# Performance work log

Hardware: AMD Instinct MI355X
Metric: run time of the kernel (lower is better)

Reference implementation:

```python
import jax, jax.numpy as jnp
import numpy as np

N = 50000
E = 400000
DIM_IN = 512
DIM_H = 64
HEADS = 8
DIM_OUT = 40
SLOPE = 0.2  # PyG GATv2Conv default negative_slope


def setup_inputs() -> dict:
    key = jax.random.key(0)
    ks = jax.random.split(key, 16)
    s = 0.05
    return {
        "x": jax.random.normal(ks[0], (N, DIM_IN), dtype=jnp.float32),
        "edge_index": jax.random.randint(ks[1], (2, E), 0, N, dtype=jnp.int64),
        "Wl1": jax.random.normal(ks[2], (DIM_IN, HEADS * DIM_H), dtype=jnp.float32) * s,
        "Wr1": jax.random.normal(ks[3], (DIM_IN, HEADS * DIM_H), dtype=jnp.float32) * s,
        "att1": jax.random.normal(ks[4], (HEADS, DIM_H), dtype=jnp.float32) * s,
        "b1": jax.random.normal(ks[5], (HEADS * DIM_H,), dtype=jnp.float32) * s,
        "Wl2": jax.random.normal(ks[6], (HEADS * DIM_H, DIM_OUT), dtype=jnp.float32) * s,
        "Wr2": jax.random.normal(ks[7], (HEADS * DIM_H, DIM_OUT), dtype=jnp.float32) * s,
        "att2": jax.random.normal(ks[8], (1, DIM_OUT), dtype=jnp.float32) * s,
        "b2": jax.random.normal(ks[9], (DIM_OUT,), dtype=jnp.float32) * s,
        "Wl3": jax.random.normal(ks[10], (HEADS * DIM_H, 2), dtype=jnp.float32) * s,
        "Wr3": jax.random.normal(ks[11], (HEADS * DIM_H, 2), dtype=jnp.float32) * s,
        "att3": jax.random.normal(ks[12], (1, 2), dtype=jnp.float32) * s,
        "b3": jax.random.normal(ks[13], (2,), dtype=jnp.float32) * s,
    }


def gatv2(x, src, dst, Wl, Wr, att, b):
    # PyG GATv2Conv: e_ij = att . LeakyReLU(W_l x_j + W_r x_i); softmax over j (by dst i);
    # out_i = sum_j alpha_ij * (W_l x_j); heads concatenated; bias added after.
    n = x.shape[0]
    H, F = att.shape
    xl = (x @ Wl).reshape(n, H, F)  # source transform
    xr = (x @ Wr).reshape(n, H, F)  # target transform
    e = jax.nn.leaky_relu(xl[src] + xr[dst], negative_slope=SLOPE)  # [E, H, F]
    logits = jnp.einsum("ehf,hf->eh", e, att)  # [E, H]
    m = jax.ops.segment_max(logits, dst, num_segments=n)  # self-loops => every segment nonempty
    ex = jnp.exp(logits - m[dst])
    denom = jax.ops.segment_sum(ex, dst, num_segments=n)
    alpha = ex / denom[dst]  # [E, H]
    out = jax.ops.segment_sum(xl[src] * alpha[:, :, None], dst, num_segments=n)  # [N, H, F]
    return out.reshape(n, H * F) + b


def reference(x, edge_index, Wl1, Wr1, att1, b1, Wl2, Wr2, att2, b2, Wl3, Wr3, att3, b3):
    # add self loops (PyG default add_self_loops=True)
    loops = jnp.arange(N, dtype=edge_index.dtype)
    ei = jnp.concatenate([edge_index, jnp.stack([loops, loops])], axis=1)
    src, dst = ei[0], ei[1]
    # eval mode: dropout is identity; ReverseLayerF is identity in forward
    h = jax.nn.relu(gatv2(x, src, dst, Wl1, Wr1, att1, b1))
    y_class = gatv2(h, src, dst, Wl2, Wr2, att2, b2)
    y_domain = gatv2(h, src, dst, Wl3, Wr3, att3, b3)
    return (y_class, y_domain)
```

## Files before the change

### kernel.cpp

```cpp
#include <hip/hip_runtime.h>
#include <math.h>

typedef unsigned short u16;
typedef unsigned int   u32;
typedef __attribute__((ext_vector_type(8))) short bf16x8;
typedef __attribute__((ext_vector_type(4))) float f32x4;
typedef __attribute__((ext_vector_type(4))) u32   u32x4;

__device__ __forceinline__ float b2f(u16 u) {
  union { u32 i; float f; } v; v.i = ((u32)u) << 16; return v.f;
}
__device__ __forceinline__ u16 f2b(float f) {
  union { u32 i; float f; } v; v.f = f;
  u32 r = v.i + 0x7FFFu + ((v.i >> 16) & 1u);
  return (u16)(r >> 16);
}
__device__ __forceinline__ float blo(u32 w) {
  union { u32 i; float f; } v; v.i = w << 16; return v.f;
}
__device__ __forceinline__ float bhi(u32 w) {
  union { u32 i; float f; } v; v.i = w & 0xFFFF0000u; return v.f;
}
__device__ __forceinline__ void ld_lds16(const u16* g, u16* l) {
  __builtin_amdgcn_global_load_lds((const __attribute__((address_space(1))) void*)g,
                                   (__attribute__((address_space(3))) void*)l, 16, 0, 0);
}

#define NN 50000
#define NE 400000
#define NT 450000
#define NBLK_SCAN 196

__global__ void k_detect(const void* x, const void* ei, int* flags) {
  __shared__ int cnt[2];
  int t = threadIdx.x;
  if (t < 2) cnt[t] = 0;
  __syncthreads();
  u16 u = ((const u16*)x)[t];
  int e = (u >> 7) & 0xFF;
  if (u == 0 || (e >= 90 && e <= 134)) atomicAdd(&cnt[0], 1);
  if (t < 16) {
    if (((const int*)ei)[2 * t + 1] == 0) atomicAdd(&cnt[1], 1);
  }
  __syncthreads();
  if (t == 0) {
    flags[0] = (cnt[0] >= 110) ? 1 : 0;
    flags[1] = (cnt[1] >= 15) ? 1 : 0;
  }
}

__device__ __forceinline__ int eidx(const int* ei, int pos, int i64) {
  return i64 ? ei[2 * pos] : ei[pos];
}

__global__ void k_convert_x(const void* x, const int* flags, u16* xb) {
  if (flags[0]) return;
  int c = blockIdx.x * 256 + threadIdx.x;
  const float* xf = (const float*)x + (size_t)c * 8;
  u32x4 o;
  #pragma unroll
  for (int i = 0; i < 4; ++i) {
    u32 lo = f2b(xf[2 * i]);
    u32 hi = f2b(xf[2 * i + 1]);
    o[i] = lo | (hi << 16);
  }
  *(u32x4*)(xb + (size_t)c * 8) = o;
}

__global__ void k_pack_w1t(const void* Wl1, const void* Wr1, const int* flags, u16* w1t) {
  int t = blockIdx.x * 256 + threadIdx.x;
  int k = t >> 10;
  int c = t & 1023;
  const void* W = (c < 512) ? Wl1 : Wr1;
  int cc = c & 511;
  u16 v;
  if (flags[0]) v = ((const u16*)W)[k * 512 + cc];
  else          v = f2b(((const float*)W)[k * 512 + cc]);
  w1t[c * 512 + k] = v;
}

__global__ void k_pack_w23t(const void* Wl2, const void* Wr2, const void* Wl3, const void* Wr3,
                            const int* flags, u16* w23t) {
  int t = blockIdx.x * 256 + threadIdx.x;
  int k = t / 96;
  int c = t % 96;
  const void* W = nullptr; int idx = 0;
  if (c < 40)      { W = Wl2; idx = k * 40 + c; }
  else if (c < 42) { W = Wl3; idx = k * 2 + (c - 40); }
  else if (c < 82) { W = Wr2; idx = k * 40 + (c - 42); }
  else if (c < 84) { W = Wr3; idx = k * 2 + (c - 82); }
  u16 v = 0;
  if (W) {
    if (flags[0]) v = ((const u16*)W)[idx];
    else          v = f2b(((const float*)W)[idx]);
  }
  w23t[c * 512 + k] = v;
}

__global__ void k_pack_params(const void* att1, const void* b1, const void* att2, const void* b2,
                              const void* att3, const void* b3, const int* flags, float* params) {
  int t = blockIdx.x * 256 + threadIdx.x;
  if (t >= 1108) return;
  const void* src; int idx;
  if (t < 512)       { src = att1; idx = t; }
  else if (t < 1024) { src = b1;   idx = t - 512; }
  else if (t < 1064) { src = att2; idx = t - 1024; }
  else if (t < 1104) { src = b2;   idx = t - 1064; }
  else if (t < 1106) { src = att3; idx = t - 1104; }
  else               { src = b3;   idx = t - 1106; }
  params[t] = flags[0] ? b2f(((const u16*)src)[idx]) : ((const float*)src)[idx];
}

__global__ void k_hist(const int* ei, const int* flags, int* deg) {
  int e = blockIdx.x * 256 + threadIdx.x;
  if (e >= NE) return;
  int d = eidx(ei, NE + e, flags[1]);
  atomicAdd(&deg[d], 1);
}

__global__ void k_scanA(const int* deg, int* row_ptr, int* bsum) {
  __shared__ int sh[256];
  int b = blockIdx.x, t = threadIdx.x;
  int i = b * 256 + t;
  int val = (i < NN) ? deg[i] + 1 : 0;
  sh[t] = val;
  __syncthreads();
  #pragma unroll
  for (int off = 1; off < 256; off <<= 1) {
    int v = (t >= off) ? sh[t - off] : 0;
    __syncthreads();
    sh[t] += v;
    __syncthreads();
  }
  if (i < NN) row_ptr[i] = sh[t] - val;
  if (t == 255) bsum[b] = sh[255];
}

__global__ void k_scanB(int* bsum, int* row_ptr) {
  __shared__ int sh[256];
  int t = threadIdx.x;
  int val = (t < NBLK_SCAN) ? bsum[t] : 0;
  sh[t] = val;
  __syncthreads();
  #pragma unroll
  for (int off = 1; off < 256; off <<= 1) {
    int v = (t >= off) ? sh[t - off] : 0;
    __syncthreads();
    sh[t] += v;
    __syncthreads();
  }
  if (t < NBLK_SCAN) bsum[t] = sh[t] - val;
  if (t == 255) row_ptr[NN] = sh[255];
}

__global__ void k_scanC(const int* bsum, int* row_ptr, int* cursor) {
  int i = blockIdx.x * 256 + threadIdx.x;
  if (i < NN) {
    int v = row_ptr[i] + bsum[blockIdx.x];
    row_ptr[i] = v;
    cursor[i] = v;
  }
}

__global__ void k_scatter(const int* ei, const int* flags, int* cursor, int* csr_src) {
  int t = blockIdx.x * 256 + threadIdx.x;
  if (t >= NT) return;
  int i64 = flags[1];
  int s, d;
  if (t < NE) { s = eidx(ei, t, i64); d = eidx(ei, NE + t, i64); }
  else        { s = d = t - NE; }
  int pos = atomicAdd(&cursor[d], 1);
  csr_src[pos] = s;
}

__global__ __launch_bounds__(256) void k_gemm1(const void* __restrict__ xraw, const u16* __restrict__ xb,
                                               const u16* __restrict__ Bt, const int* __restrict__ flags,
                                               u16* __restrict__ XL, u16* __restrict__ XR) {
  __shared__ __align__(16) u16 As[128 * 32];
  __shared__ __align__(16) u16 Bs[128 * 32];
  const int id  = blockIdx.x;
  const int xcd = id & 7;
  const int lb  = id >> 3;
  const int mt  = xcd * 49 + (lb >> 3);
  const int nt  = lb & 7;
  if (mt >= 391) return;
  const int m0 = mt * 128;
  const int n0 = nt * 128;
  const u16* __restrict__ A = flags[0] ? (const u16*)xraw : xb;
  const int t = threadIdx.x;
  const int wave = t >> 6;
  const int lane = t & 63;
  const int wm = (wave >> 1) * 64;
  const int wn = (wave & 1) * 64;
  const int fr = lane & 15;
  const int fk = lane >> 4;
  const int rsub = lane >> 2;
  const int achk = ((lane & 3) + (rsub >> 1)) & 3;
  const int sA = ((fk - (fr >> 1)) & 3) * 8;
  f32x4 acc[4][4] = {};
  for (int k0 = 0; k0 < 512; k0 += 32) {
    #pragma unroll
    for (int c = 0; c < 2; ++c) {
      int rbase = wave * 16 + c * 64;
      int gm = m0 + rbase + rsub;
      if (gm > NN - 1) gm = NN - 1;
      ld_lds16(&A[(size_t)gm * 512 + k0 + achk * 8], &As[rbase * 32]);
      ld_lds16(&Bt[(size_t)(n0 + rbase + rsub) * 512 + k0 + achk * 8], &Bs[rbase * 32]);
    }
    __syncthreads();
    bf16x8 af[4], bb[4];
    #pragma unroll
    for (int i = 0; i < 4; ++i) af[i] = *(const bf16x8*)&As[(wm + i * 16 + fr) * 32 + sA];
    #pragma unroll
    for (int j = 0; j < 4; ++j) bb[j] = *(const bf16x8*)&Bs[(wn + j * 16 + fr) * 32 + sA];
    #pragma unroll
    for (int i = 0; i < 4; ++i)
      #pragma unroll
      for (int j = 0; j < 4; ++j)
        acc[i][j] = __builtin_amdgcn_mfma_f32_16x16x32_bf16(af[i], bb[j], acc[i][j], 0, 0, 0);
    __syncthreads();
  }
  #pragma unroll
  for (int i = 0; i < 4; ++i) {
    #pragma unroll
    for (int r = 0; r < 4; ++r) {
      int gm = m0 + wm + i * 16 + fk * 4 + r;
      if (gm < NN) {
        #pragma unroll
        for (int j = 0; j < 4; ++j) {
          int gn = n0 + wn + j * 16 + fr;
          u16 v = f2b(acc[i][j][r]);
          if (gn < 512) XL[(size_t)gm * 512 + gn] = v;
          else          XR[(size_t)gm * 512 + gn - 512] = v;
        }
      }
    }
  }
}

__global__ __launch_bounds__(256) void k_gemm2(const u16* __restrict__ A, const u16* __restrict__ Bt,
                                               float* __restrict__ C) {
  __shared__ __align__(16) short As[128][40];
  __shared__ __align__(16) short Bs[96][40];
  const int m0 = blockIdx.x * 128;
  const int t = threadIdx.x;
  const int wave = t >> 6;
  const int lane = t & 63;
  const int fr = lane & 15;
  const int fk = lane >> 4;
  const int wm = wave * 32;
  f32x4 acc[2][6] = {};
  for (int k0 = 0; k0 < 512; k0 += 32) {
    #pragma unroll
    for (int h = 0; h < 2; ++h) {
      int c = t + h * 256;
      int row = c >> 2, kc = (c & 3) * 8;
      int gm = m0 + row;
      u32x4 va = {0, 0, 0, 0};
      if (gm < NN) va = *(const u32x4*)&A[(size_t)gm * 512 + k0 + kc];
      *(u32x4*)&As[row][kc] = va;
    }
    for (int c = t; c < 384; c += 256) {
      int row = c >> 2, kc = (c & 3) * 8;
      *(u32x4*)&Bs[row][kc] = *(const u32x4*)&Bt[row * 512 + k0 + kc];
    }
    __syncthreads();
    bf16x8 af[2], bb[6];
    #pragma unroll
    for (int i = 0; i < 2; ++i) af[i] = *(const bf16x8*)&As[wm + i * 16 + fr][fk * 8];
    #pragma unroll
    for (int j = 0; j < 6; ++j) bb[j] = *(const bf16x8*)&Bs[j * 16 + fr][fk * 8];
    #pragma unroll
    for (int i = 0; i < 2; ++i)
      #pragma unroll
      for (int j = 0; j < 6; ++j)
        acc[i][j] = __builtin_amdgcn_mfma_f32_16x16x32_bf16(af[i], bb[j], acc[i][j], 0, 0, 0);
    __syncthreads();
  }
  #pragma unroll
  for (int i = 0; i < 2; ++i) {
    #pragma unroll
    for (int j = 0; j < 6; ++j) {
      int gn = j * 16 + fr;
      if (gn < 84) {
        #pragma unroll
        for (int r = 0; r < 4; ++r) {
          int gm = m0 + wm + i * 16 + fk * 4 + r;
          if (gm < NN) C[(size_t)gm * 84 + gn] = acc[i][j][r];
        }
      }
    }
  }
}

__global__ __launch_bounds__(256) void k_layer1f(const u16* __restrict__ xl1, const u16* __restrict__ xr1,
                                                 const int* __restrict__ row_ptr, const int* __restrict__ csr_src,
                                                 const float* __restrict__ params, u16* __restrict__ hb) {
  int wid = blockIdx.x * 4 + (threadIdx.x >> 6);
  int lane = threadIdx.x & 63;
  int nw = gridDim.x * 4;
  float att[8];
  #pragma unroll
  for (int k = 0; k < 8; ++k) att[k] = params[lane * 8 + k];
  for (int i = wid; i < NN; i += nw) {
    int e0 = row_ptr[i], e1 = row_ptr[i + 1];
    u32x4 xrv = *(const u32x4*)&xr1[(size_t)i * 512 + lane * 8];
    float xr[8];
    #pragma unroll
    for (int q = 0; q < 4; ++q) { xr[2 * q] = blo(xrv[q]); xr[2 * q + 1] = bhi(xrv[q]); }
    float s = 0.f;
    float acc[8] = {0.f, 0.f, 0.f, 0.f, 0.f, 0.f, 0.f, 0.f};
    for (int p = e0; p < e1; p += 4) {
      int p1 = p + 1 < e1 ? p + 1 : e1 - 1;
      int p2 = p + 2 < e1 ? p + 2 : e1 - 1;
      int p3 = p + 3 < e1 ? p + 3 : e1 - 1;
      int j0 = csr_src[p], j1 = csr_src[p1], j2 = csr_src[p2], j3 = csr_src[p3];
      u32x4 v0 = *(const u32x4*)&xl1[(size_t)j0 * 512 + lane * 8];
      u32x4 v1 = *(const u32x4*)&xl1[(size_t)j1 * 512 + lane * 8];
      u32x4 v2 = *(const u32x4*)&xl1[(size_t)j2 * 512 + lane * 8];
      u32x4 v3 = *(const u32x4*)&xl1[(size_t)j3 * 512 + lane * 8];
      float m1 = (p + 1 < e1) ? 1.f : 0.f;
      float m2 = (p + 2 < e1) ? 1.f : 0.f;
      float m3 = (p + 3 < e1) ? 1.f : 0.f;
      float c0 = 0.f, c1 = 0.f, c2 = 0.f, c3 = 0.f;
      float xlv0[8], xlv1[8], xlv2[8], xlv3[8];
      #pragma unroll
      for (int q = 0; q < 4; ++q) {
        xlv0[2 * q] = blo(v0[q]); xlv0[2 * q + 1] = bhi(v0[q]);
        xlv1[2 * q] = blo(v1[q]); xlv1[2 * q + 1] = bhi(v1[q]);
        xlv2[2 * q] = blo(v2[q]); xlv2[2 * q + 1] = bhi(v2[q]);
        xlv3[2 * q] = blo(v3[q]); xlv3[2 * q + 1] = bhi(v3[q]);
      }
      #pragma unroll
      for (int k = 0; k < 8; ++k) {
        float t0 = xlv0[k] + xr[k];
        float t1 = xlv1[k] + xr[k];
        float t2 = xlv2[k] + xr[k];
        float t3 = xlv3[k] + xr[k];
        c0 = fmaf(att[k], fmaxf(t0, 0.2f * t0), c0);
        c1 = fmaf(att[k], fmaxf(t1, 0.2f * t1), c1);
        c2 = fmaf(att[k], fmaxf(t2, 0.2f * t2), c2);
        c3 = fmaf(att[k], fmaxf(t3, 0.2f * t3), c3);
      }
      c0 += __shfl_xor(c0, 1, 64); c1 += __shfl_xor(c1, 1, 64);
      c2 += __shfl_xor(c2, 1, 64); c3 += __shfl_xor(c3, 1, 64);
      c0 += __shfl_xor(c0, 2, 64); c1 += __shfl_xor(c1, 2, 64);
      c2 += __shfl_xor(c2, 2, 64); c3 += __shfl_xor(c3, 2, 64);
      c0 += __shfl_xor(c0, 4, 64); c1 += __shfl_xor(c1, 4, 64);
      c2 += __shfl_xor(c2, 4, 64); c3 += __shfl_xor(c3, 4, 64);
      float pv0 = __expf(fminf(fmaxf(c0, -30.f), 30.f));
      float pv1 = __expf(fminf(fmaxf(c1, -30.f), 30.f)) * m1;
      float pv2 = __expf(fminf(fmaxf(c2, -30.f), 30.f)) * m2;
      float pv3 = __expf(fminf(fmaxf(c3, -30.f), 30.f)) * m3;
      s += (pv0 + pv1) + (pv2 + pv3);
      #pragma unroll
      for (int k = 0; k < 8; ++k) {
        float a = fmaf(pv0, xlv0[k], pv1 * xlv1[k]);
        float b = fmaf(pv2, xlv2[k], pv3 * xlv3[k]);
        acc[k] += a + b;
      }
    }
    float r = 1.f / s;
    u32x4 o;
    #pragma unroll
    for (int q = 0; q < 4; ++q) {
      u32 lo = f2b(fmaxf(fmaf(acc[2 * q],     r, params[512 + lane * 8 + 2 * q]),     0.f));
      u32 hi = f2b(fmaxf(fmaf(acc[2 * q + 1], r, params[512 + lane * 8 + 2 * q + 1]), 0.f));
      o[q] = lo | (hi << 16);
    }
    *(u32x4*)&hb[(size_t)i * 512 + lane * 8] = o;
  }
}

__global__ __launch_bounds__(256) void k_layer23f(const float* __restrict__ xlr23, const int* __restrict__ row_ptr,
                                                  const int* __restrict__ csr_src, const float* __restrict__ params,
                                                  const int* __restrict__ flags, void* __restrict__ out) {
  int wid = blockIdx.x * 4 + (threadIdx.x >> 6);
  int lane = threadIdx.x & 63;
  int nw = gridDim.x * 4;
  int c = lane;
  bool act = c < 42;
  float att = 0.f;
  if (c < 40)      att = params[1024 + c];
  else if (c < 42) att = params[1104 + (c - 40)];
  int isbf = flags[0];
  for (int i = wid; i < NN; i += nw) {
    int e0 = row_ptr[i], e1 = row_ptr[i + 1];
    float xr = act ? xlr23[(size_t)i * 84 + 42 + c] : 0.f;
    float s2 = 0.f, s3 = 0.f, acc = 0.f;
    for (int p = e0; p < e1; p += 2) {
      int p1 = p + 1 < e1 ? p + 1 : e1 - 1;
      float m1 = (p + 1 < e1) ? 1.f : 0.f;
      int j0 = csr_src[p], j1 = csr_src[p1];
      float xl0 = act ? xlr23[(size_t)j0 * 84 + c] : 0.f;
      float xl1 = act ? xlr23[(size_t)j1 * 84 + c] : 0.f;
      float t0 = xl0 + xr, t1 = xl1 + xr;
      float v0 = att * fmaxf(t0, 0.2f * t0);
      float v1 = att * fmaxf(t1, 0.2f * t1);
      float w0 = (c < 40) ? v0 : 0.f;
      float w1 = (c < 40) ? v1 : 0.f;
      #pragma unroll
      for (int o = 32; o >= 1; o >>= 1) { w0 += __shfl_xor(w0, o, 64); w1 += __shfl_xor(w1, o, 64); }
      float u0 = v0 + __shfl_xor(v0, 1, 64);
      float u1 = v1 + __shfl_xor(v1, 1, 64);
      float l3_0 = __shfl(u0, 40, 64);
      float l3_1 = __shfl(u1, 40, 64);
      float p2_0 = __expf(fminf(fmaxf(w0, -30.f), 30.f));
      float p2_1 = __expf(fminf(fmaxf(w1, -30.f), 30.f)) * m1;
      float p3_0 = __expf(fminf(fmaxf(l3_0, -30.f), 30.f));
      float p3_1 = __expf(fminf(fmaxf(l3_1, -30.f), 30.f)) * m1;
      s2 += p2_0 + p2_1;
      s3 += p3_0 + p3_1;
      float a0 = (c < 40) ? p2_0 : p3_0;
      float a1 = (c < 40) ? p2_1 : p3_1;
      acc += fmaf(a0, xl0, a1 * xl1);
    }
    if (c < 40) {
      float v = acc / s2 + params[1064 + c];
      size_t o = (size_t)i * 40 + c;
      if (isbf) ((u16*)out)[o] = f2b(v); else ((float*)out)[o] = v;
    } else if (c < 42) {
      float v = acc / s3 + params[1106 + (c - 40)];
      size_t o = 2000000 + (size_t)i * 2 + (c - 40);
      if (isbf) ((u16*)out)[o] = f2b(v); else ((float*)out)[o] = v;
    }
  }
}

extern "C" void kernel_launch(void* const* d_in, const int* in_sizes, int n_in,
                              void* d_out, int out_size, void* d_ws, size_t ws_size,
                              hipStream_t stream) {
  const void* x    = d_in[0];
  const int*  ei   = (const int*)d_in[1];
  const void* Wl1  = d_in[2];
  const void* Wr1  = d_in[3];
  const void* att1 = d_in[4];
  const void* b1   = d_in[5];
  const void* Wl2  = d_in[6];
  const void* Wr2  = d_in[7];
  const void* att2 = d_in[8];
  const void* b2   = d_in[9];
  const void* Wl3  = d_in[10];
  const void* Wr3  = d_in[11];
  const void* att3 = d_in[12];
  const void* b3   = d_in[13];
  (void)in_sizes; (void)n_in; (void)out_size;

  char* ws = (char*)d_ws;
  size_t off = 0;
  auto alloc = [&](size_t bytes) -> void* {
    void* p = ws + off;
    off = (off + bytes + 255) & ~(size_t)255;
    return p;
  };
  int*   flags   = (int*)  alloc(64);
  u16*   xb      = (u16*)  alloc((size_t)NN * 512 * 2);
  u16*   w1t     = (u16*)  alloc((size_t)1024 * 512 * 2);
  u16*   xl1     = (u16*)  alloc((size_t)NN * 512 * 2);
  u16*   xr1     = (u16*)  alloc((size_t)NN * 512 * 2);
  u16*   hb      = (u16*)  alloc((size_t)NN * 512 * 2);
  u16*   w23t    = (u16*)  alloc((size_t)96 * 512 * 2);
  float* xlr23   = (float*)alloc((size_t)NN * 84 * 4);
  float* params  = (float*)alloc(1108 * 4);
  int*   row_ptr = (int*)  alloc((NN + 1) * 4);
  int*   deg     = (int*)  alloc(NN * 4);
  int*   cursor  = (int*)  alloc(NN * 4);
  int*   csr_src = (int*)  alloc((NT + 16) * 4);
  int*   bsum    = (int*)  alloc(256 * 4);
  if (ws_size < off) return;

  hipLaunchKernelGGL(k_detect, dim3(1), dim3(128), 0, stream, x, (const void*)ei, flags);
  hipLaunchKernelGGL(k_convert_x, dim3(12500), dim3(256), 0, stream, x, flags, xb);
  hipLaunchKernelGGL(k_pack_w1t, dim3(2048), dim3(256), 0, stream, Wl1, Wr1, flags, w1t);
  hipLaunchKernelGGL(k_pack_w23t, dim3(192), dim3(256), 0, stream, Wl2, Wr2, Wl3, Wr3, flags, w23t);
  hipLaunchKernelGGL(k_pack_params, dim3(5), dim3(256), 0, stream, att1, b1, att2, b2, att3, b3, flags, params);
  hipMemsetAsync(deg, 0, NN * 4, stream);
  hipLaunchKernelGGL(k_hist, dim3((NE + 255) / 256), dim3(256), 0, stream, ei, flags, deg);
  hipLaunchKernelGGL(k_scanA, dim3(NBLK_SCAN), dim3(256), 0, stream, deg, row_ptr, bsum);
  hipLaunchKernelGGL(k_scanB, dim3(1), dim3(256), 0, stream, bsum, row_ptr);
  hipLaunchKernelGGL(k_scanC, dim3(NBLK_SCAN), dim3(256), 0, stream, bsum, row_ptr, cursor);
  hipLaunchKernelGGL(k_scatter, dim3((NT + 255) / 256), dim3(256), 0, stream, ei, flags, cursor, csr_src);
  hipLaunchKernelGGL(k_gemm1, dim3(3136), dim3(256), 0, stream, x, xb, w1t, flags, xl1, xr1);
  hipLaunchKernelGGL(k_layer1f, dim3(4096), dim3(256), 0, stream, xl1, xr1, row_ptr, csr_src, params, hb);
  hipLaunchKernelGGL(k_gemm2, dim3(391), dim3(256), 0, stream, hb, w23t, xlr23);
  hipLaunchKernelGGL(k_layer23f, dim3(4096), dim3(256), 0, stream, xlr23, row_ptr, csr_src, params, flags, d_out);
}
```

Baseline: 479.5 us.

## Fuse prep kernels, inline dtype detection, single-block scan, bf16 layer-2 features

Merges input conversion, weight packing, parameter packing and degree zeroing into one kernel. Dtype and index-width detection move into each kernel via wave ballots, replacing the flags buffer. The three-pass scan becomes one 1024-thread block. gemm1 keeps B fragments in registers with a 64-wide K step, and the layer-2/3 projection buffer is stored as bf16 to halve gather bandwidth. This trades some precision in the final layers and serialises the scan on one block.

After: 626.8 us. +30.7%, slower.

```diff
diff --git a/kernel.cpp b/kernel.cpp
--- a/kernel.cpp
+++ b/kernel.cpp
@@ -26,158 +26,154 @@
                                    (__attribute__((address_space(3))) void*)l, 16, 0, 0);
 }
 
+__device__ __forceinline__ int is_bf16_w(const void* x) {
+  int lane = threadIdx.x & 63;
+  u32 w = ((const u32*)x)[lane];
+  u16 a = (u16)(w & 0xFFFF), b = (u16)(w >> 16);
+  int ea = (a >> 7) & 0xFF, eb = (b >> 7) & 0xFF;
+  bool oka = (a == 0) || (ea >= 90 && ea <= 134);
+  bool okb = (b == 0) || (eb >= 90 && eb <= 134);
+  int cnt = (int)__popcll(__ballot(oka)) + (int)__popcll(__ballot(okb));
+  return cnt >= 110;
+}
+__device__ __forceinline__ int is_i64_w(const int* ei) {
+  int lane = threadIdx.x & 63;
+  int v = (lane < 16) ? (ei[2 * lane + 1] == 0) : 0;
+  return (int)__popcll(__ballot(v)) >= 15;
+}
+
 #define NN 50000
 #define NE 400000
 #define NT 450000
-#define NBLK_SCAN 196
-
-__global__ void k_detect(const void* x, const void* ei, int* flags) {
-  __shared__ int cnt[2];
-  int t = threadIdx.x;
-  if (t < 2) cnt[t] = 0;
-  __syncthreads();
-  u16 u = ((const u16*)x)[t];
-  int e = (u >> 7) & 0xFF;
-  if (u == 0 || (e >= 90 && e <= 134)) atomicAdd(&cnt[0], 1);
-  if (t < 16) {
-    if (((const int*)ei)[2 * t + 1] == 0) atomicAdd(&cnt[1], 1);
-  }
-  __syncthreads();
-  if (t == 0) {
-    flags[0] = (cnt[0] >= 110) ? 1 : 0;
-    flags[1] = (cnt[1] >= 15) ? 1 : 0;
-  }
-}
-
-__device__ __forceinline__ int eidx(const int* ei, int pos, int i64) {
-  return i64 ? ei[2 * pos] : ei[pos];
-}
-
-__global__ void k_convert_x(const void* x, const int* flags, u16* xb) {
-  if (flags[0]) return;
-  int c = blockIdx.x * 256 + threadIdx.x;
-  const float* xf = (const float*)x + (size_t)c * 8;
-  u32x4 o;
-  #pragma unroll
-  for (int i = 0; i < 4; ++i) {
-    u32 lo = f2b(xf[2 * i]);
-    u32 hi = f2b(xf[2 * i + 1]);
-    o[i] = lo | (hi << 16);
-  }
-  *(u32x4*)(xb + (size_t)c * 8) = o;
-}
-
-__global__ void k_pack_w1t(const void* Wl1, const void* Wr1, const int* flags, u16* w1t) {
-  int t = blockIdx.x * 256 + threadIdx.x;
-  int k = t >> 10;
-  int c = t & 1023;
-  const void* W = (c < 512) ? Wl1 : Wr1;
-  int cc = c & 511;
-  u16 v;
-  if (flags[0]) v = ((const u16*)W)[k * 512 + cc];
-  else          v = f2b(((const float*)W)[k * 512 + cc]);
-  w1t[c * 512 + k] = v;
-}
-
-__global__ void k_pack_w23t(const void* Wl2, const void* Wr2, const void* Wl3, const void* Wr3,
-                            const int* flags, u16* w23t) {
-  int t = blockIdx.x * 256 + threadIdx.x;
-  int k = t / 96;
-  int c = t % 96;
-  const void* W = nullptr; int idx = 0;
-  if (c < 40)      { W = Wl2; idx = k * 40 + c; }
-  else if (c < 42) { W = Wl3; idx = k * 2 + (c - 40); }
-  else if (c < 82) { W = Wr2; idx = k * 40 + (c - 42); }
-  else if (c < 84) { W = Wr3; idx = k * 2 + (c - 82); }
-  u16 v = 0;
-  if (W) {
-    if (flags[0]) v = ((const u16*)W)[idx];
-    else          v = f2b(((const float*)W)[idx]);
-  }
-  w23t[c * 512 + k] = v;
-}
-
-__global__ void k_pack_params(const void* att1, const void* b1, const void* att2, const void* b2,
-                              const void* att3, const void* b3, const int* flags, float* params) {
-  int t = blockIdx.x * 256 + threadIdx.x;
-  if (t >= 1108) return;
-  const void* src; int idx;
-  if (t < 512)       { src = att1; idx = t; }
-  else if (t < 1024) { src = b1;   idx = t - 512; }
-  else if (t < 1064) { src = att2; idx = t - 1024; }
-  else if (t < 1104) { src = b2;   idx = t - 1064; }
-  else if (t < 1106) { src = att3; idx = t - 1104; }
-  else               { src = b3;   idx = t - 1106; }
-  params[t] = flags[0] ? b2f(((const u16*)src)[idx]) : ((const float*)src)[idx];
-}
-
-__global__ void k_hist(const int* ei, const int* flags, int* deg) {
+
+__global__ void k_prep(const void* x,
+                       const void* Wl1, const void* Wr1,
+                       const void* Wl2, const void* Wr2, const void* Wl3, const void* Wr3,
+                       const void* att1, const void* b1, const void* att2, const void* b2,
+                       const void* att3, const void* b3,
+                       u16* xb, u16* w1t, u16* w23t, float* params, int* deg) {
+  const int b = blockIdx.x;
+  const int t = threadIdx.x;
+  const int isbf = is_bf16_w(x);
+  if (!isbf) {
+    int c = b * 256 + t;
+    const float* xf = (const float*)x + (size_t)c * 8;
+    u32x4 o;
+    #pragma unroll
+    for (int i = 0; i < 4; ++i) {
+      u32 lo = f2b(xf[2 * i]);
+      u32 hi = f2b(xf[2 * i + 1]);
+      o[i] = lo | (hi << 16);
+    }
+    *(u32x4*)(xb + (size_t)c * 8) = o;
+  }
+  if (b < 2048) {
+    int tt = b * 256 + t;
+    int k = tt >> 10, c = tt & 1023;
+    const void* W = (c < 512) ? Wl1 : Wr1;
+    int cc = c & 511;
+    u16 v = isbf ? ((const u16*)W)[k * 512 + cc] : f2b(((const float*)W)[k * 512 + cc]);
+    w1t[c * 512 + k] = v;
+  } else if (b < 2240) {
+    int tt = (b - 2048) * 256 + t;
+    int k = tt / 96, c = tt % 96;
+    const void* W = nullptr; int idx = 0;
+    if (c < 40)      { W = Wl2; idx = k * 40 + c; }
+    else if (c < 42) { W = Wl3; idx = k * 2 + (c - 40); }
+    else if (c < 82) { W = Wr2; idx = k * 40 + (c - 42); }
+    else if (c < 84) { W = Wr3; idx = k * 2 + (c - 82); }
+    u16 v = 0;
+    if (W) v = isbf ? ((const u16*)W)[idx] : f2b(((const float*)W)[idx]);
+    w23t[c * 512 + k] = v;
+  } else if (b < 2245) {
+    int tt = (b - 2240) * 256 + t;
+    if (tt < 1108) {
+      const void* src; int idx;
+      if (tt < 512)       { src = att1; idx = tt; }
+      else if (tt < 1024) { src = b1;   idx = tt - 512; }
+      else if (tt < 1064) { src = att2; idx = tt - 1024; }
+      else if (tt < 1104) { src = b2;   idx = tt - 1064; }
+      else if (tt < 1106) { src = att3; idx = tt - 1104; }
+      else                { src = b3;   idx = tt - 1106; }
+      params[tt] = isbf ? b2f(((const u16*)src)[idx]) : ((const float*)src)[idx];
+    }
+  } else if (b < 2441) {
+    int i = (b - 2245) * 256 + t;
+    if (i < NN) deg[i] = 0;
+  }
+}
+
+__global__ void k_hist(const int* ei, int* deg) {
+  int i64 = is_i64_w(ei);
   int e = blockIdx.x * 256 + threadIdx.x;
   if (e >= NE) return;
-  int d = eidx(ei, NE + e, flags[1]);
+  int d = i64 ? ei[2 * (NE + e)] : ei[NE + e];
   atomicAdd(&deg[d], 1);
 }
 
-__global__ void k_scanA(const int* deg, int* row_ptr, int* bsum) {
-  __shared__ int sh[256];
-  int b = blockIdx.x, t = threadIdx.x;
-  int i = b * 256 + t;
-  int val = (i < NN) ? deg[i] + 1 : 0;
-  sh[t] = val;
+__global__ __launch_bounds__(1024) void k_scan(const int* __restrict__ deg, int* __restrict__ row_ptr,
+                                               int* __restrict__ cursor) {
+  __shared__ int wsum[16];
+  int t = threadIdx.x;
+  int lane = t & 63, wid = t >> 6;
+  int base = t * 49;
+  int s = 0;
+  for (int q = 0; q < 49; ++q) {
+    int i = base + q;
+    s += (i < NN) ? deg[i] + 1 : 0;
+  }
+  int incl = s;
+  #pragma unroll
+  for (int o = 1; o < 64; o <<= 1) {
+    int u = __shfl_up(incl, o, 64);
+    if (lane >= o) incl += u;
+  }
+  if (lane == 63) wsum[wid] = incl;
   __syncthreads();
-  #pragma unroll
-  for (int off = 1; off < 256; off <<= 1) {
-    int v = (t >= off) ? sh[t - off] : 0;
-    __syncthreads();
-    sh[t] += v;
-    __syncthreads();
-  }
-  if (i < NN) row_ptr[i] = sh[t] - val;
-  if (t == 255) bsum[b] = sh[255];
-}
-
-__global__ void k_scanB(int* bsum, int* row_ptr) {
-  __shared__ int sh[256];
-  int t = threadIdx.x;
-  int val = (t < NBLK_SCAN) ? bsum[t] : 0;
-  sh[t] = val;
+  if (wid == 0) {
+    int v = (lane < 16) ? wsum[lane] : 0;
+    int iv = v;
+    #pragma unroll
+    for (int o = 1; o < 16; o <<= 1) {
+      int u = __shfl_up(iv, o, 64);
+      if (lane >= o) iv += u;
+    }
+    if (lane < 16) wsum[lane] = iv - v;
+  }
   __syncthreads();
-  #pragma unroll
-  for (int off = 1; off < 256; off <<= 1) {
-    int v = (t >= off) ? sh[t - off] : 0;
-    __syncthreads();
-    sh[t] += v;
-    __syncthreads();
-  }
-  if (t < NBLK_SCAN) bsum[t] = sh[t] - val;
-  if (t == 255) row_ptr[NN] = sh[255];
-}
-
-__global__ void k_scanC(const int* bsum, int* row_ptr, int* cursor) {
-  int i = blockIdx.x * 256 + threadIdx.x;
-  if (i < NN) {
-    int v = row_ptr[i] + bsum[blockIdx.x];
-    row_ptr[i] = v;
-    cursor[i] = v;
-  }
-}
-
-__global__ void k_scatter(const int* ei, const int* flags, int* cursor, int* csr_src) {
+  int run = wsum[wid] + incl - s;
+  for (int q = 0; q < 49; ++q) {
+    int i = base + q;
+    if (i < NN) {
+      row_ptr[i] = run;
+      cursor[i] = run;
+      run += deg[i] + 1;
+    }
+  }
+  if (t == 1023) row_ptr[NN] = run;
+}
+
+__global__ void k_scatter(const int* ei, int* cursor, int* csr_src) {
+  int i64 = is_i64_w(ei);
   int t = blockIdx.x * 256 + threadIdx.x;
   if (t >= NT) return;
-  int i64 = flags[1];
   int s, d;
-  if (t < NE) { s = eidx(ei, t, i64); d = eidx(ei, NE + t, i64); }
-  else        { s = d = t - NE; }
+  if (t < NE) {
+    s = i64 ? ei[2 * t] : ei[t];
+    d = i64 ? ei[2 * (NE + t)] : ei[NE + t];
+  } else {
+    s = d = t - NE;
+  }
   int pos = atomicAdd(&cursor[d], 1);
   csr_src[pos] = s;
 }
 
 __global__ __launch_bounds__(256) void k_gemm1(const void* __restrict__ xraw, const u16* __restrict__ xb,
-                                               const u16* __restrict__ Bt, const int* __restrict__ flags,
+                                               const u16* __restrict__ Bt,
                                                u16* __restrict__ XL, u16* __restrict__ XR) {
-  __shared__ __align__(16) u16 As[128 * 32];
-  __shared__ __align__(16) u16 Bs[128 * 32];
+  __shared__ __align__(16) u16 As0[128 * 32];
+  __shared__ __align__(16) u16 As1[128 * 32];
+  const int isbf = is_bf16_w(xraw);
   const int id  = blockIdx.x;
   const int xcd = id & 7;
   const int lb  = id >> 3;
@@ -186,7 +182,7 @@
   if (mt >= 391) return;
   const int m0 = mt * 128;
   const int n0 = nt * 128;
-  const u16* __restrict__ A = flags[0] ? (const u16*)xraw : xb;
+  const u16* __restrict__ A = isbf ? (const u16*)xraw : xb;
   const int t = threadIdx.x;
   const int wave = t >> 6;
   const int lane = t & 63;
@@ -197,28 +193,47 @@
   const int rsub = lane >> 2;
   const int achk = ((lane & 3) + (rsub >> 1)) & 3;
   const int sA = ((fk - (fr >> 1)) & 3) * 8;
+  const u16* Brow = Bt + (size_t)(n0 + wn + fr) * 512 + fk * 8;
   f32x4 acc[4][4] = {};
-  for (int k0 = 0; k0 < 512; k0 += 32) {
+  bf16x8 bb0[4], bb1[4];
+  #pragma unroll
+  for (int j = 0; j < 4; ++j) {
+    bb0[j] = *(const bf16x8*)(Brow + (size_t)(j * 16) * 512);
+    bb1[j] = *(const bf16x8*)(Brow + (size_t)(j * 16) * 512 + 32);
+  }
+  for (int k0 = 0; k0 < 512; k0 += 64) {
     #pragma unroll
     for (int c = 0; c < 2; ++c) {
       int rbase = wave * 16 + c * 64;
       int gm = m0 + rbase + rsub;
       if (gm > NN - 1) gm = NN - 1;
-      ld_lds16(&A[(size_t)gm * 512 + k0 + achk * 8], &As[rbase * 32]);
-      ld_lds16(&Bt[(size_t)(n0 + rbase + rsub) * 512 + k0 + achk * 8], &Bs[rbase * 32]);
+      ld_lds16(&A[(size_t)gm * 512 + k0 + achk * 8], &As0[rbase * 32]);
+      ld_lds16(&A[(size_t)gm * 512 + (k0 + 32) + achk * 8], &As1[rbase * 32]);
     }
     __syncthreads();
-    bf16x8 af[4], bb[4];
-    #pragma unroll
-    for (int i = 0; i < 4; ++i) af[i] = *(const bf16x8*)&As[(wm + i * 16 + fr) * 32 + sA];
-    #pragma unroll
-    for (int j = 0; j < 4; ++j) bb[j] = *(const bf16x8*)&Bs[(wn + j * 16 + fr) * 32 + sA];
+    bf16x8 af0[4], af1[4];
+    #pragma unroll
+    for (int i = 0; i < 4; ++i) af0[i] = *(const bf16x8*)&As0[(wm + i * 16 + fr) * 32 + sA];
+    #pragma unroll
+    for (int i = 0; i < 4; ++i) af1[i] = *(const bf16x8*)&As1[(wm + i * 16 + fr) * 32 + sA];
     #pragma unroll
     for (int i = 0; i < 4; ++i)
       #pragma unroll
       for (int j = 0; j < 4; ++j)
-        acc[i][j] = __builtin_amdgcn_mfma_f32_16x16x32_bf16(af[i], bb[j], acc[i][j], 0, 0, 0);
+        acc[i][j] = __builtin_amdgcn_mfma_f32_16x16x32_bf16(af0[i], bb0[j], acc[i][j], 0, 0, 0);
+    #pragma unroll
+    for (int i = 0; i < 4; ++i)
+      #pragma unroll
+      for (int j = 0; j < 4; ++j)
+        acc[i][j] = __builtin_amdgcn_mfma_f32_16x16x32_bf16(af1[i], bb1[j], acc[i][j], 0, 0, 0);
     __syncthreads();
+    if (k0 + 64 < 512) {
+      #pragma unroll
+      for (int j = 0; j < 4; ++j) {
+        bb0[j] = *(const bf16x8*)(Brow + (size_t)(j * 16) * 512 + (k0 + 64));
+        bb1[j] = *(const bf16x8*)(Brow + (size_t)(j * 16) * 512 + (k0 + 96));
+      }
+    }
   }
   #pragma unroll
   for (int i = 0; i < 4; ++i) {
@@ -239,7 +254,7 @@
 }
 
 __global__ __launch_bounds__(256) void k_gemm2(const u16* __restrict__ A, const u16* __restrict__ Bt,
-                                               float* __restrict__ C) {
+                                               u16* __restrict__ C) {
   __shared__ __align__(16) short As[128][40];
   __shared__ __align__(16) short Bs[96][40];
   const int m0 = blockIdx.x * 128;
@@ -286,7 +301,7 @@
         #pragma unroll
         for (int r = 0; r < 4; ++r) {
           int gm = m0 + wm + i * 16 + fk * 4 + r;
-          if (gm < NN) C[(size_t)gm * 84 + gn] = acc[i][j][r];
+          if (gm < NN) C[(size_t)gm * 84 + gn] = f2b(acc[i][j][r]);
         }
       }
     }
@@ -372,9 +387,10 @@
   }
 }
 
-__global__ __launch_bounds__(256) void k_layer23f(const float* __restrict__ xlr23, const int* __restrict__ row_ptr,
-                                                  const int* __restrict__ csr_src, const float* __restrict__ params,
-                                                  const int* __restrict__ flags, void* __restrict__ out) {
+__global__ __launch_bounds__(256) void k_layer23f(const void* __restrict__ xref, const u16* __restrict__ xlr23,
+                                                  const int* __restrict__ row_ptr, const int* __restrict__ csr_src,
+                                                  const float* __restrict__ params, void* __restrict__ out) {
+  int isbf = is_bf16_w(xref);
   int wid = blockIdx.x * 4 + (threadIdx.x >> 6);
   int lane = threadIdx.x & 63;
   int nw = gridDim.x * 4;
@@ -383,17 +399,16 @@
   float att = 0.f;
   if (c < 40)      att = params[1024 + c];
   else if (c < 42) att = params[1104 + (c - 40)];
-  int isbf = flags[0];
   for (int i = wid; i < NN; i += nw) {
     int e0 = row_ptr[i], e1 = row_ptr[i + 1];
-    float xr = act ? xlr23[(size_t)i * 84 + 42 + c] : 0.f;
+    float xr = act ? b2f(xlr23[(size_t)i * 84 + 42 + c]) : 0.f;
     float s2 = 0.f, s3 = 0.f, acc = 0.f;
     for (int p = e0; p < e1; p += 2) {
       int p1 = p + 1 < e1 ? p + 1 : e1 - 1;
       float m1 = (p + 1 < e1) ? 1.f : 0.f;
       int j0 = csr_src[p], j1 = csr_src[p1];
-      float xl0 = act ? xlr23[(size_t)j0 * 84 + c] : 0.f;
-      float xl1 = act ? xlr23[(size_t)j1 * 84 + c] : 0.f;
+      float xl0 = act ? b2f(xlr23[(size_t)j0 * 84 + c]) : 0.f;
+      float xl1 = act ? b2f(xlr23[(size_t)j1 * 84 + c]) : 0.f;
       float t0 = xl0 + xr, t1 = xl1 + xr;
       float v0 = att * fmaxf(t0, 0.2f * t0);
       float v1 = att * fmaxf(t1, 0.2f * t1);
@@ -453,35 +468,28 @@
     off = (off + bytes + 255) & ~(size_t)255;
     return p;
   };
-  int*   flags   = (int*)  alloc(64);
   u16*   xb      = (u16*)  alloc((size_t)NN * 512 * 2);
   u16*   w1t     = (u16*)  alloc((size_t)1024 * 512 * 2);
   u16*   xl1     = (u16*)  alloc((size_t)NN * 512 * 2);
   u16*   xr1     = (u16*)  alloc((size_t)NN * 512 * 2);
   u16*   hb      = (u16*)  alloc((size_t)NN * 512 * 2);
   u16*   w23t    = (u16*)  alloc((size_t)96 * 512 * 2);
-  float* xlr23   = (float*)alloc((size_t)NN * 84 * 4);
+  u16*   xlr23   = (u16*)  alloc((size_t)NN * 84 * 2);
   float* params  = (float*)alloc(1108 * 4);
   int*   row_ptr = (int*)  alloc((NN + 1) * 4);
   int*   deg     = (int*)  alloc(NN * 4);
   int*   cursor  = (int*)  alloc(NN * 4);
   int*   csr_src = (int*)  alloc((NT + 16) * 4);
-  int*   bsum    = (int*)  alloc(256 * 4);
   if (ws_size < off) return;
 
-  hipLaunchKernelGGL(k_detect, dim3(1), dim3(128), 0, stream, x, (const void*)ei, flags);
-  hipLaunchKernelGGL(k_convert_x, dim3(12500), dim3(256), 0, stream, x, flags, xb);
-  hipLaunchKernelGGL(k_pack_w1t, dim3(2048), dim3(256), 0, stream, Wl1, Wr1, flags, w1t);
-  hipLaunchKernelGGL(k_pack_w23t, dim3(192), dim3(256), 0, stream, Wl2, Wr2, Wl3, Wr3, flags, w23t);
-  hipLaunchKernelGGL(k_pack_params, dim3(5), dim3(256), 0, stream, att1, b1, att2, b2, att3, b3, flags, params);
-  hipMemsetAsync(deg, 0, NN * 4, stream);
-  hipLaunchKernelGGL(k_hist, dim3((NE + 255) / 256), dim3(256), 0, stream, ei, flags, deg);
-  hipLaunchKernelGGL(k_scanA, dim3(NBLK_SCAN), dim3(256), 0, stream, deg, row_ptr, bsum);
-  hipLaunchKernelGGL(k_scanB, dim3(1), dim3(256), 0, stream, bsum, row_ptr);
-  hipLaunchKernelGGL(k_scanC, dim3(NBLK_SCAN), dim3(256), 0, stream, bsum, row_ptr, cursor);
-  hipLaunchKernelGGL(k_scatter, dim3((NT + 255) / 256), dim3(256), 0, stream, ei, flags, cursor, csr_src);
-  hipLaunchKernelGGL(k_gemm1, dim3(3136), dim3(256), 0, stream, x, xb, w1t, flags, xl1, xr1);
+  hipLaunchKernelGGL(k_prep, dim3(12500), dim3(256), 0, stream,
+                     x, Wl1, Wr1, Wl2, Wr2, Wl3, Wr3, att1, b1, att2, b2, att3, b3,
+                     xb, w1t, w23t, params, deg);
+  hipLaunchKernelGGL(k_hist, dim3((NE + 255) / 256), dim3(256), 0, stream, ei, deg);
+  hipLaunchKernelGGL(k_scan, dim3(1), dim3(1024), 0, stream, deg, row_ptr, cursor);
+  hipLaunchKernelGGL(k_scatter, dim3((NT + 255) / 256), dim3(256), 0, stream, ei, cursor, csr_src);
+  hipLaunchKernelGGL(k_gemm1, dim3(3136), dim3(256), 0, stream, x, xb, w1t, xl1, xr1);
   hipLaunchKernelGGL(k_layer1f, dim3(4096), dim3(256), 0, stream, xl1, xr1, row_ptr, csr_src, params, hb);
   hipLaunchKernelGGL(k_gemm2, dim3(391), dim3(256), 0, stream, hb, w23t, xlr23);
-  hipLaunchKernelGGL(k_layer23f, dim3(4096), dim3(256), 0, stream, xlr23, row_ptr, csr_src, params, flags, d_out);
-}
+  hipLaunchKernelGGL(k_layer23f, dim3(4096), dim3(256), 0, stream, x, xlr23, row_ptr, csr_src, params, d_out);
+}
```
